# Performance work log

Hardware: AMD Instinct MI355X
Metric: run time of the kernel (lower is better)

## Reference

```python
import jax, jax.numpy as jnp
import numpy as np

B, H, W, Q, E, M, K, WIN = 4, 192, 192, 160, 96, 96, 4, 7
NO_ELECTRON_WEIGHT = 0.1


def _bce_logits(x, z):
    # binary_cross_entropy_with_logits, elementwise: softplus(x) - x*z
    return jnp.logaddexp(0.0, x) - x * z


def setup_inputs() -> dict:
    key = jax.random.key(0)
    ks = jax.random.split(key, 11)
    is_electron_logit = jax.random.normal(ks[0], (B * Q,), jnp.float32)
    true_segmap = jax.random.uniform(ks[1], (B, H, W, E), jnp.float32)
    binary_mask_logits = jax.random.normal(ks[2], (B, H, W, Q), jnp.float32)
    portion_logits = jax.random.normal(ks[3], (B, H, W, Q), jnp.float32)
    # keep incidence points away from borders so the 7x7 window stays in-bounds
    incidence_points = jax.random.uniform(ks[4], (B, E, 2), jnp.float32) * (H - 8) + 4.0
    positions = jax.random.uniform(ks[5], (B, Q, 2), jnp.float32) * H
    a = jax.random.normal(ks[6], (B, Q, 3), jnp.float32)
    l00 = jax.nn.softplus(a[..., 0]) + 0.1
    l11 = jax.nn.softplus(a[..., 2]) + 0.1
    l10 = 0.5 * a[..., 1]
    zero = jnp.zeros_like(l00)
    chol = jnp.stack([jnp.stack([l00, zero], -1), jnp.stack([l10, l11], -1)], -2)  # [B,Q,2,2] lower-tri
    occupancy_logits = jax.random.normal(ks[7], (B, H, W, K), jnp.float32)
    occupancy_true = jax.random.randint(ks[8], (B, H, W), 0, K, jnp.int32)
    qkeys = jax.random.split(ks[9], B)
    matched_q = jnp.stack([jax.random.permutation(k, Q)[:M] for k in qkeys]).astype(jnp.int32)
    ekeys = jax.random.split(ks[10], B)
    matched_e = jnp.stack([jax.random.permutation(k, E) for k in ekeys]).astype(jnp.int32)
    return dict(is_electron_logit=is_electron_logit, true_segmap=true_segmap,
                binary_mask_logits=binary_mask_logits, portion_logits=portion_logits,
                incidence_points=incidence_points, positions=positions, chol=chol,
                occupancy_logits=occupancy_logits, occupancy_true=occupancy_true,
                matched_q=matched_q, matched_e=matched_e)


def reference(is_electron_logit, true_segmap, binary_mask_logits, portion_logits,
              incidence_points, positions, chol, occupancy_logits, occupancy_true,
              matched_q, matched_e):
    # ---- class loss (weighted BCE over flat per-query logits) ----
    labels = jnp.zeros((B * Q,), is_electron_logit.dtype)
    glob = (jnp.arange(B)[:, None] * Q + matched_q).reshape(-1)
    labels = labels.at[glob].set(1.0)
    weights = jnp.where(labels > 0, 1.0, NO_ELECTRON_WEIGHT).astype(is_electron_logit.dtype)
    class_loss = jnp.mean(weights * _bce_logits(is_electron_logit, labels))

    # ---- reorder segmentation maps to matched order (_reorder_segmentation_map) ----
    true_r = jnp.take_along_axis(true_segmap, matched_e[:, None, None, :], axis=3)        # [B,H,W,M]
    bin_r = jnp.take_along_axis(binary_mask_logits, matched_q[:, None, None, :], axis=3)  # [B,H,W,M]
    por_r = jnp.take_along_axis(portion_logits, matched_q[:, None, None, :], axis=3)      # [B,H,W,M]

    # ---- mask BCE on 7x7 windows around floor(matched incidence point) ----
    pts_r = jnp.take_along_axis(incidence_points, matched_e[..., None], axis=1)  # [B,M,2]
    pix = jnp.floor(pts_r).astype(jnp.int32)
    half = WIN // 2
    dr = jnp.arange(-half, half + 1)
    rows = pix[..., 0][:, :, None, None] + dr[None, None, :, None]  # [B,M,7,1]
    cols = pix[..., 1][:, :, None, None] + dr[None, None, None, :]  # [B,M,1,7]
    bi = jnp.arange(B)[:, None, None, None]
    mi = jnp.arange(M)[None, :, None, None]
    tv = true_r[bi, rows, cols, mi]  # [B,M,7,7]
    lg = bin_r[bi, rows, cols, mi]
    bce_loss = jnp.mean(_bce_logits(lg, tv))

    # ---- dice loss (softmax over matched-electron dim) ----
    portion = jax.nn.softmax(por_r, axis=-1)
    num = jnp.sum(2.0 * true_r * portion, axis=(1, 2, 3))
    den = jnp.sum(true_r + portion, axis=(1, 2, 3))
    dice_loss = jnp.mean(1.0 - (num + 1.0) / (den + 1.0))

    # ---- distance NLL (2D MVN with lower-tri scale) ----
    centers_r = jnp.take_along_axis(positions, matched_q[..., None], axis=1)       # [B,M,2]
    chol_r = jnp.take_along_axis(chol, matched_q[..., None, None], axis=1)         # [B,M,2,2]
    d = pts_r - centers_r
    z0 = d[..., 0] / chol_r[..., 0, 0]
    z1 = (d[..., 1] - chol_r[..., 1, 0] * z0) / chol_r[..., 1, 1]
    nll = 0.5 * (z0 * z0 + z1 * z1) + jnp.log(2.0 * jnp.pi) \
          + jnp.log(chol_r[..., 0, 0]) + jnp.log(chol_r[..., 1, 1])
    nll = jnp.where(jnp.isinf(nll), 1e7, nll)
    nll_loss = jnp.mean(nll)

    # ---- occupancy loss (per-pixel electron-count cross-entropy) ----
    logp = jax.nn.log_softmax(occupancy_logits, axis=-1)
    occ_loss = -jnp.mean(jnp.take_along_axis(logp, occupancy_true[..., None], axis=-1))

    # loss_weights all 1.0 (defaults); dot(weights, terms)
    return class_loss + bce_loss + dice_loss + nll_loss + occ_loss
```

## Files before the change

kernel.cpp:

```cpp
#include <hip/hip_runtime.h>
#include <math.h>

#define B_ 4
#define H_ 192
#define W_ 192
#define Q_ 160
#define E_ 96
#define M_ 96
#define HW_ (H_ * W_)
#define NPIX_ (B_ * HW_)
#define TPIX 16
#define TILES_PER_BLK 9
#define NDICE 1024
#define NSMALL 962
#define NBUCKET 64
#define WS_NUM0 4
#define WS_TS0  260
#define WS_TOTAL 516

#define POR_BYTES (TPIX * Q_ * 4)
#define TRU_BYTES (TPIX * E_ * 4)
#define TILE_BYTES (POR_BYTES + TRU_BYTES)
#define POR_F (TPIX * Q_)

__device__ __forceinline__ void stage16(const void* g, void* l) {
    __builtin_amdgcn_global_load_lds(
        (const __attribute__((address_space(1))) void*)g,
        (__attribute__((address_space(3))) void*)l, 16, 0, 0);
}

template <int CTRL, int RMASK>
__device__ __forceinline__ float dpp_add_step(float x) {
    int v = __builtin_amdgcn_update_dpp(0, __float_as_int(x), CTRL, RMASK, 0xF, false);
    return x + __int_as_float(v);
}
__device__ __forceinline__ float wave_sum63(float x) {
    x = dpp_add_step<0x111, 0xF>(x);
    x = dpp_add_step<0x112, 0xF>(x);
    x = dpp_add_step<0x114, 0xF>(x);
    x = dpp_add_step<0x118, 0xF>(x);
    x = dpp_add_step<0x142, 0xA>(x);
    x = dpp_add_step<0x143, 0xC>(x);
    return x;
}

__device__ __forceinline__ float waveSumAll(float v) {
    for (int m = 32; m > 0; m >>= 1) v += __shfl_xor(v, m, 64);
    return v;
}

__device__ __forceinline__ float softplusf(float x) {
    return fmaxf(x, 0.f) + log1pf(__expf(-fabsf(x)));
}

__global__ __launch_bounds__(256) void fused_kernel(
    const float* __restrict__ logit,
    const float* __restrict__ trueseg,
    const float* __restrict__ binlog,
    const float* __restrict__ por,
    const float* __restrict__ inc,
    const float* __restrict__ pos,
    const float* __restrict__ chol,
    const float* __restrict__ occlog,
    const int* __restrict__ occtrue,
    const int* __restrict__ mqall,
    const int* __restrict__ meall,
    float* __restrict__ ws)
{
    __shared__ float tilebuf[2 * TILE_BYTES / 4];
    __shared__ float sA[4], sT[4];
    const int tid  = threadIdx.x;
    const int lane = tid & 63;
    const int wid  = tid >> 6;
    const int blk  = blockIdx.x;

    if (blk < NDICE) {
        const int b = blk >> 8;
        const int slot = blk & 255;
        const bool hi = lane < 32;
        const int* mq = mqall + b * M_;
        const int* me = meall + b * M_;
        const int mqa = mq[lane];
        const int mea = me[lane];
        int mqb = 0, meb = 0;
        if (hi) { mqb = mq[64 + lane]; meb = me[64 + lane]; }
        const char* porb = (const char*)(por + (size_t)b * HW_ * Q_);
        const char* trb  = (const char*)(trueseg + (size_t)b * HW_ * E_);

        float an = 0.f;
        float at = 0.f;

        {
            const int p0 = slot * TPIX;
            const char* gp = porb + (size_t)p0 * (Q_ * 4);
            const char* gt = trb  + (size_t)p0 * (E_ * 4);
            #pragma unroll
            for (int i = 0; i < 4; ++i) {
                const int off = i * 4096 + wid * 1024;
                const char* src = (off < POR_BYTES) ? (gp + off)
                                                    : (gt + (off - POR_BYTES));
                stage16(src + lane * 16, (char*)tilebuf + off);
            }
        }

        int bufsel = 0;
        for (int t = 0; t < TILES_PER_BLK; ++t) {
            __syncthreads();
            if (t + 1 < TILES_PER_BLK) {
                const int p0 = (slot + (t + 1) * 256) * TPIX;
                const char* gp = porb + (size_t)p0 * (Q_ * 4);
                const char* gt = trb  + (size_t)p0 * (E_ * 4);
                const int nb = bufsel ^ 1;
                #pragma unroll
                for (int i = 0; i < 4; ++i) {
                    const int off = i * 4096 + wid * 1024;
                    const char* src = (off < POR_BYTES) ? (gp + off)
                                                        : (gt + (off - POR_BYTES));
                    stage16(src + lane * 16, (char*)tilebuf + nb * TILE_BYTES + off);
                }
            }
            const float* pl = tilebuf + bufsel * (TILE_BYTES / 4);
            const float* tl = pl + POR_F;
            #pragma unroll
            for (int k = 0; k < 4; ++k) {
                const int pix = wid * 4 + k;
                float p0v = pl[pix * Q_ + mqa];
                float t0  = tl[pix * E_ + mea];
                float e1 = 0.f, se1 = 0.f, t1 = 0.f;
                if (hi) {
                    float p1 = pl[pix * Q_ + mqb];
                    t1 = tl[pix * E_ + meb];
                    e1 = __expf(p1);
                    se1 = t1 * e1;
                }
                float e0 = __expf(p0v);
                float s  = wave_sum63(e0 + e1);
                float se = wave_sum63(t0 * e0 + se1);
                an += __fdividef(se, s);
                at += t0 + t1;
            }
            bufsel ^= 1;
        }
        float atr = wave_sum63(at);
        if (lane == 63) { sA[wid] = an; sT[wid] = atr; }
        __syncthreads();
        if (tid == 0) {
            float num = sA[0] + sA[1] + sA[2] + sA[3];
            float ts  = sT[0] + sT[1] + sT[2] + sT[3];
            int bucket = blk & (NBUCKET - 1);
            atomicAdd(&ws[WS_NUM0 + bucket * 4 + b], 2.f * num);
            atomicAdd(&ws[WS_TS0  + bucket * 4 + b], ts);
        }
    } else {
        float* red = tilebuf;
        float* lab = tilebuf + 256;
        const int s = blk - NDICE;
        float acc = 0.f;
        if (s == 0) {
            for (int i = tid; i < B_ * Q_; i += 256) lab[i] = 0.f;
            __syncthreads();
            for (int i = tid; i < B_ * M_; i += 256) {
                int b = i / M_;
                lab[b * Q_ + mqall[i]] = 1.f;
            }
            __syncthreads();
            for (int i = tid; i < B_ * Q_; i += 256) {
                float x = logit[i];
                float z = lab[i];
                float w = z > 0.f ? 1.f : 0.1f;
                acc += w * (softplusf(x) - x * z);
            }
            red[tid] = acc; __syncthreads();
            for (int st = 128; st > 0; st >>= 1) { if (tid < st) red[tid] += red[tid + st]; __syncthreads(); }
            if (tid == 0) ws[0] = red[0];
        } else if (s == 1) {
            for (int i = tid; i < B_ * M_; i += 256) {
                int b = i / M_;
                int qi = mqall[i];
                int ei = meall[i];
                float px = inc[(b * E_ + ei) * 2 + 0];
                float py = inc[(b * E_ + ei) * 2 + 1];
                float cx = pos[(b * Q_ + qi) * 2 + 0];
                float cy = pos[(b * Q_ + qi) * 2 + 1];
                const float* ch = chol + (size_t)(b * Q_ + qi) * 4;
                float l00 = ch[0], l10 = ch[2], l11 = ch[3];
                float d0 = px - cx, d1 = py - cy;
                float z0 = d0 / l00;
                float z1 = (d1 - l10 * z0) / l11;
                float nll = 0.5f * (z0 * z0 + z1 * z1) + 1.837877066409345f
                            + logf(l00) + logf(l11);
                if (isinf(nll)) nll = 1e7f;
                acc += nll;
            }
            red[tid] = acc; __syncthreads();
            for (int st = 128; st > 0; st >>= 1) { if (tid < st) red[tid] += red[tid + st]; __syncthreads(); }
            if (tid == 0) ws[2] = red[0];
        } else if (s < 386) {
            int idx = s - 2;
            int b = idx / M_;
            int ei = meall[idx];
            int qi = mqall[idx];
            float px = inc[(b * E_ + ei) * 2 + 0];
            float py = inc[(b * E_ + ei) * 2 + 1];
            int r0 = (int)floorf(px) - 3;
            int c0 = (int)floorf(py) - 3;
            if (tid < 49) {
                int rr = r0 + tid / 7;
                int cc = c0 + tid % 7;
                size_t pix = ((size_t)b * H_ + rr) * W_ + cc;
                float tv = trueseg[pix * E_ + ei];
                float lg = binlog[pix * Q_ + qi];
                acc = softplusf(lg) - lg * tv;
            }
            red[tid] = acc; __syncthreads();
            for (int st = 128; st > 0; st >>= 1) { if (tid < st) red[tid] += red[tid + st]; __syncthreads(); }
            if (tid == 0) atomicAdd(&ws[1], red[0]);
        } else {
            int p = (s - 386) * 256 + tid;
            if (p < NPIX_) {
                float4 v = *(const float4*)(occlog + (size_t)p * 4);
                int lb = occtrue[p];
                float m = fmaxf(fmaxf(v.x, v.y), fmaxf(v.z, v.w));
                float lse = m + __logf(__expf(v.x - m) + __expf(v.y - m) +
                                       __expf(v.z - m) + __expf(v.w - m));
                float xs = lb == 0 ? v.x : (lb == 1 ? v.y : (lb == 2 ? v.z : v.w));
                acc = lse - xs;
            }
            red[tid] = acc; __syncthreads();
            for (int st = 128; st > 0; st >>= 1) { if (tid < st) red[tid] += red[tid + st]; __syncthreads(); }
            if (tid == 0) atomicAdd(&ws[3], red[0]);
        }
    }
}

__global__ __launch_bounds__(64) void final_kernel(const float* __restrict__ ws,
                                                   float* __restrict__ out)
{
    const int lane = threadIdx.x;
    float n[B_], t[B_];
    for (int b = 0; b < B_; ++b) {
        n[b] = waveSumAll(ws[WS_NUM0 + lane * 4 + b]);
        t[b] = waveSumAll(ws[WS_TS0  + lane * 4 + b]);
    }
    if (lane == 0) {
        float class_l = ws[0] * (1.f / (B_ * Q_));
        float bce_l   = ws[1] * (1.f / (B_ * M_ * 49));
        float nll_l   = ws[2] * (1.f / (B_ * M_));
        float occ_l   = ws[3] * (1.f / NPIX_);
        float dice = 0.f;
        for (int b = 0; b < B_; ++b)
            dice += 1.f - (n[b] + 1.f) / (t[b] + (float)HW_ + 1.f);
        dice *= (1.f / B_);
        out[0] = class_l + bce_l + nll_l + occ_l + dice;
    }
}

extern "C" void kernel_launch(void* const* d_in, const int* in_sizes, int n_in,
                              void* d_out, int out_size, void* d_ws, size_t ws_size,
                              hipStream_t stream) {
    const float* logit   = (const float*)d_in[0];
    const float* trueseg = (const float*)d_in[1];
    const float* binlog  = (const float*)d_in[2];
    const float* por     = (const float*)d_in[3];
    const float* inc     = (const float*)d_in[4];
    const float* pos     = (const float*)d_in[5];
    const float* chol    = (const float*)d_in[6];
    const float* occlog  = (const float*)d_in[7];
    const int*   occtrue = (const int*)d_in[8];
    const int*   mq      = (const int*)d_in[9];
    const int*   me      = (const int*)d_in[10];
    float* out = (float*)d_out;
    float* ws  = (float*)d_ws;

    (void)hipMemsetAsync(d_ws, 0, WS_TOTAL * sizeof(float), stream);

    hipLaunchKernelGGL(fused_kernel, dim3(NDICE + NSMALL), dim3(256), 0, stream,
                       logit, trueseg, binlog, por, inc, pos, chol, occlog, occtrue,
                       mq, me, ws);
    hipLaunchKernelGGL(final_kernel, dim3(1), dim3(64), 0, stream, ws, out);
}
```

Baseline: 245.1 us.

## Replace block-wide double buffer with per-wave 8-deep LDS ring and wave reductions

```diff
diff --git a/kernel.cpp b/kernel.cpp
--- a/kernel.cpp
+++ b/kernel.cpp
@@ -9,8 +9,6 @@
 #define M_ 96
 #define HW_ (H_ * W_)
 #define NPIX_ (B_ * HW_)
-#define TPIX 16
-#define TILES_PER_BLK 9
 #define NDICE 1024
 #define NSMALL 962
 #define NBUCKET 64
@@ -18,15 +16,26 @@
 #define WS_TS0  260
 #define WS_TOTAL 516
 
-#define POR_BYTES (TPIX * Q_ * 4)
-#define TRU_BYTES (TPIX * E_ * 4)
-#define TILE_BYTES (POR_BYTES + TRU_BYTES)
-#define POR_F (TPIX * Q_)
+#define NJOB 36
+#define RING 8
 
 __device__ __forceinline__ void stage16(const void* g, void* l) {
     __builtin_amdgcn_global_load_lds(
         (const __attribute__((address_space(1))) void*)g,
         (__attribute__((address_space(3))) void*)l, 16, 0, 0);
+}
+
+__device__ __forceinline__ void wait_vmcnt(int n) {
+    switch (n) {
+    case 0: asm volatile("s_waitcnt vmcnt(0)" ::: "memory"); break;
+    case 1: asm volatile("s_waitcnt vmcnt(1)" ::: "memory"); break;
+    case 2: asm volatile("s_waitcnt vmcnt(2)" ::: "memory"); break;
+    case 3: asm volatile("s_waitcnt vmcnt(3)" ::: "memory"); break;
+    case 4: asm volatile("s_waitcnt vmcnt(4)" ::: "memory"); break;
+    case 5: asm volatile("s_waitcnt vmcnt(5)" ::: "memory"); break;
+    case 6: asm volatile("s_waitcnt vmcnt(6)" ::: "memory"); break;
+    default: asm volatile("s_waitcnt vmcnt(7)" ::: "memory"); break;
+    }
 }
 
 template <int CTRL, int RMASK>
@@ -67,8 +76,7 @@
     const int* __restrict__ meall,
     float* __restrict__ ws)
 {
-    __shared__ float tilebuf[2 * TILE_BYTES / 4];
-    __shared__ float sA[4], sT[4];
+    __shared__ float tilebuf[4 * RING * 256];
     const int tid  = threadIdx.x;
     const int lane = tid & 63;
     const int wid  = tid >> 6;
@@ -84,76 +92,71 @@
         const int mea = me[lane];
         int mqb = 0, meb = 0;
         if (hi) { mqb = mq[64 + lane]; meb = me[64 + lane]; }
+        asm volatile("" :: "v"(mqa), "v"(mea), "v"(mqb), "v"(meb));
+
         const char* porb = (const char*)(por + (size_t)b * HW_ * Q_);
         const char* trb  = (const char*)(trueseg + (size_t)b * HW_ * E_);
+        const char* srcbase = (lane < 40) ? porb : trb;
+        const int rowbytes  = (lane < 40) ? Q_ * 4 : E_ * 4;
+        const int inrow     = (lane < 40) ? lane * 16 : (lane - 40) * 16;
+
+        char* ringb = (char*)tilebuf + wid * (RING * 1024);
 
         float an = 0.f;
         float at = 0.f;
 
-        {
-            const int p0 = slot * TPIX;
-            const char* gp = porb + (size_t)p0 * (Q_ * 4);
-            const char* gt = trb  + (size_t)p0 * (E_ * 4);
-            #pragma unroll
-            for (int i = 0; i < 4; ++i) {
-                const int off = i * 4096 + wid * 1024;
-                const char* src = (off < POR_BYTES) ? (gp + off)
-                                                    : (gt + (off - POR_BYTES));
-                stage16(src + lane * 16, (char*)tilebuf + off);
-            }
-        }
-
-        int bufsel = 0;
-        for (int t = 0; t < TILES_PER_BLK; ++t) {
-            __syncthreads();
-            if (t + 1 < TILES_PER_BLK) {
-                const int p0 = (slot + (t + 1) * 256) * TPIX;
-                const char* gp = porb + (size_t)p0 * (Q_ * 4);
-                const char* gt = trb  + (size_t)p0 * (E_ * 4);
-                const int nb = bufsel ^ 1;
-                #pragma unroll
-                for (int i = 0; i < 4; ++i) {
-                    const int off = i * 4096 + wid * 1024;
-                    const char* src = (off < POR_BYTES) ? (gp + off)
-                                                        : (gt + (off - POR_BYTES));
-                    stage16(src + lane * 16, (char*)tilebuf + nb * TILE_BYTES + off);
-                }
-            }
-            const float* pl = tilebuf + bufsel * (TILE_BYTES / 4);
-            const float* tl = pl + POR_F;
-            #pragma unroll
-            for (int k = 0; k < 4; ++k) {
-                const int pix = wid * 4 + k;
-                float p0v = pl[pix * Q_ + mqa];
-                float t0  = tl[pix * E_ + mea];
-                float e1 = 0.f, se1 = 0.f, t1 = 0.f;
-                if (hi) {
-                    float p1 = pl[pix * Q_ + mqb];
-                    t1 = tl[pix * E_ + meb];
-                    e1 = __expf(p1);
-                    se1 = t1 * e1;
-                }
-                float e0 = __expf(p0v);
-                float s  = wave_sum63(e0 + e1);
-                float se = wave_sum63(t0 * e0 + se1);
-                an += __fdividef(se, s);
-                at += t0 + t1;
-            }
-            bufsel ^= 1;
-        }
+        #define STAGE_JOB(j_) do {                                             \
+            int t_ = (j_) >> 2, k_ = (j_) & 3;                                 \
+            int pix_ = (slot + t_ * 256) * 16 + wid * 4 + k_;                  \
+            stage16(srcbase + (size_t)pix_ * rowbytes + inrow,                 \
+                    ringb + ((j_) & (RING - 1)) * 1024);                       \
+        } while (0)
+
+        #define COMPUTE_JOB(j_) do {                                           \
+            const float* row_ = tilebuf + wid * (RING * 256)                   \
+                                + ((j_) & (RING - 1)) * 256;                   \
+            float p0v_ = row_[mqa];                                            \
+            float t0_  = row_[160 + mea];                                      \
+            float e1_ = 0.f, se1_ = 0.f, t1_ = 0.f;                            \
+            if (hi) {                                                          \
+                float p1_ = row_[mqb];                                         \
+                t1_ = row_[160 + meb];                                         \
+                e1_ = __expf(p1_);                                             \
+                se1_ = t1_ * e1_;                                              \
+            }                                                                  \
+            float e0_ = __expf(p0v_);                                          \
+            float s_  = wave_sum63(e0_ + e1_);                                 \
+            float se_ = wave_sum63(t0_ * e0_ + se1_);                          \
+            an += __fdividef(se_, s_);                                         \
+            at += t0_ + t1_;          \
+        } while (0)
+
+        #pragma unroll
+        for (int j = 0; j < RING; ++j) STAGE_JOB(j);
+
+        #pragma unroll 4
+        for (int j = 0; j < NJOB - RING; ++j) {
+            asm volatile("s_waitcnt vmcnt(7)" ::: "memory");
+            COMPUTE_JOB(j);
+            STAGE_JOB(j + RING);
+        }
+
+        #pragma unroll
+        for (int j = NJOB - RING; j < NJOB; ++j) {
+            wait_vmcnt(NJOB - 1 - j);
+            COMPUTE_JOB(j);
+        }
+
         float atr = wave_sum63(at);
-        if (lane == 63) { sA[wid] = an; sT[wid] = atr; }
-        __syncthreads();
-        if (tid == 0) {
-            float num = sA[0] + sA[1] + sA[2] + sA[3];
-            float ts  = sT[0] + sT[1] + sT[2] + sT[3];
+        if (lane == 63) {
             int bucket = blk & (NBUCKET - 1);
-            atomicAdd(&ws[WS_NUM0 + bucket * 4 + b], 2.f * num);
-            atomicAdd(&ws[WS_TS0  + bucket * 4 + b], ts);
-        }
+            atomicAdd(&ws[WS_NUM0 + bucket * 4 + b], 2.f * an);
+            atomicAdd(&ws[WS_TS0  + bucket * 4 + b], atr);
+        }
+        #undef STAGE_JOB
+        #undef COMPUTE_JOB
     } else {
-        float* red = tilebuf;
-        float* lab = tilebuf + 256;
+        float* lab = tilebuf;
         const int s = blk - NDICE;
         float acc = 0.f;
         if (s == 0) {
@@ -170,9 +173,8 @@
                 float w = z > 0.f ? 1.f : 0.1f;
                 acc += w * (softplusf(x) - x * z);
             }
-            red[tid] = acc; __syncthreads();
-            for (int st = 128; st > 0; st >>= 1) { if (tid < st) red[tid] += red[tid + st]; __syncthreads(); }
-            if (tid == 0) ws[0] = red[0];
+            float wsum = wave_sum63(acc);
+            if (lane == 63) atomicAdd(&ws[0], wsum);
         } else if (s == 1) {
             for (int i = tid; i < B_ * M_; i += 256) {
                 int b = i / M_;
@@ -192,9 +194,8 @@
                 if (isinf(nll)) nll = 1e7f;
                 acc += nll;
             }
-            red[tid] = acc; __syncthreads();
-            for (int st = 128; st > 0; st >>= 1) { if (tid < st) red[tid] += red[tid + st]; __syncthreads(); }
-            if (tid == 0) ws[2] = red[0];
+            float wsum = wave_sum63(acc);
+            if (lane == 63) atomicAdd(&ws[2], wsum);
         } else if (s < 386) {
             int idx = s - 2;
             int b = idx / M_;
@@ -212,9 +213,10 @@
                 float lg = binlog[pix * Q_ + qi];
                 acc = softplusf(lg) - lg * tv;
             }
-            red[tid] = acc; __syncthreads();
-            for (int st = 128; st > 0; st >>= 1) { if (tid < st) red[tid] += red[tid + st]; __syncthreads(); }
-            if (tid == 0) atomicAdd(&ws[1], red[0]);
+            if (wid == 0) {
+                float wsum = wave_sum63(acc);
+                if (lane == 63) atomicAdd(&ws[1], wsum);
+            }
         } else {
             int p = (s - 386) * 256 + tid;
             if (p < NPIX_) {
@@ -226,9 +228,8 @@
                 float xs = lb == 0 ? v.x : (lb == 1 ? v.y : (lb == 2 ? v.z : v.w));
                 acc = lse - xs;
             }
-            red[tid] = acc; __syncthreads();
-            for (int st = 128; st > 0; st >>= 1) { if (tid < st) red[tid] += red[tid + st]; __syncthreads(); }
-            if (tid == 0) atomicAdd(&ws[3], red[0]);
+            float wsum = wave_sum63(acc);
+            if (lane == 63) atomicAdd(&ws[3], wsum);
         }
     }
 }
```

Result: slower. 262.9 us (+7.3%).
